# Optimization experiments

Measured on AMD Instinct MI355X. Metric: run time of the kernel, lower is better.

## Reference

```python
import jax, jax.numpy as jnp
import numpy as np

B, S, DIN, DOUT = 4, 2048, 4096, 4096
W_SCALE = 64.0   # makes round(weight*scale) produce non-trivial int8 values
X_SCALE = 16.0   # input_scale so x*scale truncates to non-zero int32 values


def setup_inputs() -> dict:
    key = jax.random.key(0)
    k1, k2, k3 = jax.random.split(key, 3)
    # kaiming_uniform fan_in: bound = sqrt(6/fan_in)
    bound = float(np.sqrt(6.0 / DIN))
    weight = jax.random.uniform(k1, (DOUT, DIN), jnp.float32, -bound, bound)
    x = jax.random.normal(k2, (B, S, DIN), jnp.float32)
    bias = jax.random.normal(k3, (DOUT,), jnp.float32) * 0.01
    weight_scale = jnp.full((DOUT,), W_SCALE, jnp.float32)
    input_scale = jnp.full((1,), X_SCALE, jnp.float32)
    return {"x": x, "weight": weight, "bias": bias,
            "weight_scale": weight_scale, "input_scale": input_scale}


def reference(x, weight, bias, weight_scale, input_scale):
    # x = x * input_scale (pre-scale path of forward)
    xs = x * input_scale
    # fake-quant weights: round to int8 with wraparound, like torch .to(int8)
    w_int = jnp.round(weight * weight_scale[:, None]).astype(jnp.int8)
    # x.to(torch.int32): truncation toward zero
    x_int = xs.astype(jnp.int32)
    # F.linear on the integer-valued tensors (computed in f32: values are exact ints)
    acc = jnp.einsum('bsd,od->bso', x_int.astype(jnp.float32),
                     w_int.astype(jnp.float32))
    acc = acc + bias  # bias added inside linear
    # dequant: divide by per-channel weight_scale and the scalar input_scale
    out = acc / (weight_scale * input_scale)
    return out
```

## Files before the change

kernel.cpp:

```cpp
#include <hip/hip_runtime.h>

#define GM 8192
#define GN 4096
#define GK 4096

#define BM 128
#define BN 128
#define BK 64

using int4v = __attribute__((ext_vector_type(4))) int;

__global__ __launch_bounds__(256) void quant_x_k(const float4* __restrict__ x,
                                                 unsigned int* __restrict__ xq,
                                                 const float* __restrict__ iscale,
                                                 int n4) {
    int i = blockIdx.x * blockDim.x + threadIdx.x;
    if (i >= n4) return;
    float s = *iscale;
    float4 v = x[i];
    int q0 = (int)(v.x * s);
    int q1 = (int)(v.y * s);
    int q2 = (int)(v.z * s);
    int q3 = (int)(v.w * s);
    unsigned int packed = (unsigned int)(q0 & 0xff)
                        | ((unsigned int)(q1 & 0xff) << 8)
                        | ((unsigned int)(q2 & 0xff) << 16)
                        | ((unsigned int)(q3 & 0xff) << 24);
    xq[i] = packed;
}

__global__ __launch_bounds__(256) void quant_w_k(const float4* __restrict__ w,
                                                 unsigned int* __restrict__ wq,
                                                 const float* __restrict__ wscale,
                                                 int n4) {
    int i = blockIdx.x * blockDim.x + threadIdx.x;
    if (i >= n4) return;
    int row = i >> 10;
    float s = wscale[row];
    float4 v = w[i];
    int q0 = (int)rintf(v.x * s);
    int q1 = (int)rintf(v.y * s);
    int q2 = (int)rintf(v.z * s);
    int q3 = (int)rintf(v.w * s);
    unsigned int packed = (unsigned int)(q0 & 0xff)
                        | ((unsigned int)(q1 & 0xff) << 8)
                        | ((unsigned int)(q2 & 0xff) << 16)
                        | ((unsigned int)(q3 & 0xff) << 24);
    wq[i] = packed;
}

__global__ __launch_bounds__(256) void qlinear_gemm_i8(
    const signed char* __restrict__ Aq,
    const signed char* __restrict__ Bq,
    const float* __restrict__ bias,
    const float* __restrict__ wscale,
    const float* __restrict__ iscale,
    float* __restrict__ C) {
    __shared__ signed char As[BM * BK];
    __shared__ signed char Bs[BN * BK];

    const int tid  = threadIdx.x;
    const int wave = tid >> 6;
    const int lane = tid & 63;
    const int m0 = blockIdx.x * BM;
    const int n0 = blockIdx.y * BN;
    const int wm = (wave >> 1) * 64;
    const int wn = (wave & 1) * 64;

    int4v acc[4][4];
#pragma unroll
    for (int i = 0; i < 4; ++i)
#pragma unroll
        for (int j = 0; j < 4; ++j)
            acc[i][j] = int4v{0, 0, 0, 0};

    const int seg = wave * 2;
    const int rA = m0 + seg * 16 + (lane >> 2);
    const int rB = n0 + seg * 16 + (lane >> 2);
    const signed char* gA0 = Aq + (size_t)rA * GK + (lane & 3) * 16;
    const signed char* gA1 = gA0 + (size_t)16 * GK;
    const signed char* gB0 = Bq + (size_t)rB * GK + (lane & 3) * 16;
    const signed char* gB1 = gB0 + (size_t)16 * GK;
    signed char* lA0 = As + seg * 1024 + lane * 16;
    signed char* lA1 = lA0 + 1024;
    signed char* lB0 = Bs + seg * 1024 + lane * 16;
    signed char* lB1 = lB0 + 1024;

    const int kgrp = (lane >> 4) * 16;
    const signed char* fA = As + (wm + (lane & 15)) * BK + kgrp;
    const signed char* fB = Bs + (wn + (lane & 15)) * BK + kgrp;

#define GLL16(g, l)                                                     \
    __builtin_amdgcn_global_load_lds(                                   \
        (__attribute__((address_space(1))) void*)(void*)(g),            \
        (__attribute__((address_space(3))) void*)(l), 16, 0, 0)

    for (int k0 = 0; k0 < GK; k0 += BK) {
        GLL16(gA0 + k0, lA0);
        GLL16(gA1 + k0, lA1);
        GLL16(gB0 + k0, lB0);
        GLL16(gB1 + k0, lB1);
        __syncthreads();

        int4v a[4], b[4];
#pragma unroll
        for (int i = 0; i < 4; ++i) {
            a[i] = *(const int4v*)(fA + i * 16 * BK);
            b[i] = *(const int4v*)(fB + i * 16 * BK);
        }
#pragma unroll
        for (int mi = 0; mi < 4; ++mi)
#pragma unroll
            for (int ni = 0; ni < 4; ++ni)
                acc[mi][ni] = __builtin_amdgcn_mfma_i32_16x16x64_i8(
                    a[mi], b[ni], acc[mi][ni], 0, 0, 0);
        __syncthreads();
    }

    const float isc = *iscale;
#pragma unroll
    for (int ni = 0; ni < 4; ++ni) {
        const int col = n0 + wn + ni * 16 + (lane & 15);
        const float bs = bias[col];
        const float inv = 1.0f / (wscale[col] * isc);
#pragma unroll
        for (int mi = 0; mi < 4; ++mi) {
            const int row0 = m0 + wm + mi * 16 + (lane >> 4) * 4;
#pragma unroll
            for (int r = 0; r < 4; ++r) {
                C[(size_t)(row0 + r) * GN + col] =
                    ((float)acc[mi][ni][r] + bs) * inv;
            }
        }
    }
#undef GLL16
}

extern "C" void kernel_launch(void* const* d_in, const int* in_sizes, int n_in,
                              void* d_out, int out_size, void* d_ws, size_t ws_size,
                              hipStream_t stream) {
    const float* x      = (const float*)d_in[0];
    const float* w      = (const float*)d_in[1];
    const float* bias   = (const float*)d_in[2];
    const float* wscale = (const float*)d_in[3];
    const float* iscale = (const float*)d_in[4];
    float* out = (float*)d_out;

    signed char* xq = (signed char*)d_ws;
    signed char* wq = xq + (size_t)GM * GK;

    const int n4x = GM * GK / 4;
    quant_x_k<<<n4x / 256, 256, 0, stream>>>((const float4*)x,
                                             (unsigned int*)xq, iscale, n4x);
    const int n4w = GN * GK / 4;
    quant_w_k<<<n4w / 256, 256, 0, stream>>>((const float4*)w,
                                             (unsigned int*)wq, wscale, n4w);

    dim3 grid(GM / BM, GN / BN);
    qlinear_gemm_i8<<<grid, 256, 0, stream>>>(xq, wq, bias, wscale, iscale, out);
}
```

Measured before the change: 427.3 us.

## Widen GEMM N-tile to 256 and XOR-swizzle LDS layout for int8 MFMA

Doubles the block's N tile so each wave computes a 64x128 sub-tile with 32 accumulators, which raises arithmetic intensity per LDS/global load. The global-to-LDS copy addresses and the fragment reads now use a matching XOR swizzle of the 16-byte k-chunks to cut LDS bank conflicts. A launch_bounds min-blocks hint of 2 is added. The cost is more accumulator registers per thread, which may lower occupancy, and half as many blocks in the grid.

```diff
diff --git a/kernel.cpp b/kernel.cpp
--- a/kernel.cpp
+++ b/kernel.cpp
@@ -5,7 +5,7 @@
 #define GK 4096
 
 #define BM 128
-#define BN 128
+#define BN 256
 #define BK 64
 
 using int4v = __attribute__((ext_vector_type(4))) int;
@@ -49,7 +49,7 @@
     wq[i] = packed;
 }
 
-__global__ __launch_bounds__(256) void qlinear_gemm_i8(
+__global__ __launch_bounds__(256, 2) void qlinear_gemm_i8(
     const signed char* __restrict__ Aq,
     const signed char* __restrict__ Bq,
     const float* __restrict__ bias,
@@ -65,30 +65,27 @@
     const int m0 = blockIdx.x * BM;
     const int n0 = blockIdx.y * BN;
     const int wm = (wave >> 1) * 64;
-    const int wn = (wave & 1) * 64;
+    const int wn = (wave & 1) * 128;
 
-    int4v acc[4][4];
+    int4v acc[4][8];
 #pragma unroll
     for (int i = 0; i < 4; ++i)
 #pragma unroll
-        for (int j = 0; j < 4; ++j)
+        for (int j = 0; j < 8; ++j)
             acc[i][j] = int4v{0, 0, 0, 0};
 
-    const int seg = wave * 2;
-    const int rA = m0 + seg * 16 + (lane >> 2);
-    const int rB = n0 + seg * 16 + (lane >> 2);
-    const signed char* gA0 = Aq + (size_t)rA * GK + (lane & 3) * 16;
-    const signed char* gA1 = gA0 + (size_t)16 * GK;
-    const signed char* gB0 = Bq + (size_t)rB * GK + (lane & 3) * 16;
-    const signed char* gB1 = gB0 + (size_t)16 * GK;
-    signed char* lA0 = As + seg * 1024 + lane * 16;
-    signed char* lA1 = lA0 + 1024;
-    signed char* lB0 = Bs + seg * 1024 + lane * 16;
-    signed char* lB1 = lB0 + 1024;
+    const int kcl = (((lane & 3) ^ ((lane >> 3) & 3))) * 16;
 
-    const int kgrp = (lane >> 4) * 16;
-    const signed char* fA = As + (wm + (lane & 15)) * BK + kgrp;
-    const signed char* fB = Bs + (wn + (lane & 15)) * BK + kgrp;
+    const int segA = wave * 2;
+    const signed char* gA0 = Aq + (size_t)(m0 + segA * 16 + (lane >> 2)) * GK + kcl;
+    signed char* lA0 = As + segA * 1024 + lane * 16;
+    const int segB = wave * 4;
+    const signed char* gB0 = Bq + (size_t)(n0 + segB * 16 + (lane >> 2)) * GK + kcl;
+    signed char* lB0 = Bs + segB * 1024 + lane * 16;
+
+    const int pos = ((lane >> 4) ^ ((lane >> 1) & 3)) * 16;
+    const signed char* fA = As + (wm + (lane & 15)) * BK + pos;
+    const signed char* fB = Bs + (wn + (lane & 15)) * BK + pos;
 
 #define GLL16(g, l)                                                     \
     __builtin_amdgcn_global_load_lds(                                   \
@@ -97,21 +94,24 @@
 
     for (int k0 = 0; k0 < GK; k0 += BK) {
         GLL16(gA0 + k0, lA0);
-        GLL16(gA1 + k0, lA1);
+        GLL16(gA0 + (size_t)16 * GK + k0, lA0 + 1024);
         GLL16(gB0 + k0, lB0);
-        GLL16(gB1 + k0, lB1);
+        GLL16(gB0 + (size_t)16 * GK + k0, lB0 + 1024);
+        GLL16(gB0 + (size_t)32 * GK + k0, lB0 + 2048);
+        GLL16(gB0 + (size_t)48 * GK + k0, lB0 + 3072);
         __syncthreads();
 
-        int4v a[4], b[4];
+        int4v a[4], b[8];
 #pragma unroll
-        for (int i = 0; i < 4; ++i) {
+        for (int i = 0; i < 4; ++i)
             a[i] = *(const int4v*)(fA + i * 16 * BK);
-            b[i] = *(const int4v*)(fB + i * 16 * BK);
-        }
+#pragma unroll
+        for (int j = 0; j < 8; ++j)
+            b[j] = *(const int4v*)(fB + j * 16 * BK);
 #pragma unroll
         for (int mi = 0; mi < 4; ++mi)
 #pragma unroll
-            for (int ni = 0; ni < 4; ++ni)
+            for (int ni = 0; ni < 8; ++ni)
                 acc[mi][ni] = __builtin_amdgcn_mfma_i32_16x16x64_i8(
                     a[mi], b[ni], acc[mi][ni], 0, 0, 0);
         __syncthreads();
@@ -119,7 +119,7 @@
 
     const float isc = *iscale;
 #pragma unroll
-    for (int ni = 0; ni < 4; ++ni) {
+    for (int ni = 0; ni < 8; ++ni) {
         const int col = n0 + wn + ni * 16 + (lane & 15);
         const float bs = bias[col];
         const float inv = 1.0f / (wscale[col] * isc);
```

After: 404.4 us. -5.3%, faster.
